# Performance work log

Measured on AMD Instinct MI355X. Metric: run time of the kernel, lower is better.

Reference implementation:

```python
import jax, jax.numpy as jnp
import numpy as np

NUM_SCALES = 7
WEIGHTS = [1.0] * 7


def get_m(r, c):
    # r, c: [B, H, W] float coords; density map is [B, a, a], a = min(H, W)
    B, H, W = r.shape
    a = min(H, W)
    N = H * W
    xf = jnp.clip(jnp.floor(r), 0, a - 1).astype(jnp.int32)
    yf = jnp.clip(jnp.floor(c), 0, a - 1).astype(jnp.int32)
    xc = jnp.clip(jnp.ceil(r), 0, a - 1).astype(jnp.int32)
    yc = jnp.clip(jnp.ceil(c), 0, a - 1).astype(jnp.int32)
    xw = r - xf.astype(r.dtype)
    yw = c - yf.astype(c.dtype)
    w_tl = (1 - xw) * (1 - yw)
    w_tr = xw * (1 - yw)
    w_bl = (1 - xw) * yw
    w_br = xw * yw
    idx = jnp.concatenate([
        (xf * a + yf).reshape(B, N), (xc * a + yf).reshape(B, N),
        (xf * a + yc).reshape(B, N), (xc * a + yc).reshape(B, N)], axis=1)
    w = jnp.concatenate([
        w_tl.reshape(B, N), w_tr.reshape(B, N),
        w_bl.reshape(B, N), w_br.reshape(B, N)], axis=1)
    dm = jnp.zeros((B, a * a), dtype=r.dtype)
    dm = dm.at[jnp.arange(B)[:, None], idx].add(w)
    return dm.reshape(B, a, a)


def masked_bce(pred, tgt):
    # torch F.binary_cross_entropy clamps log terms at -100
    p = pred.reshape(-1)
    t = tgt.reshape(-1)
    log_p = jnp.clip(jnp.log(p), -100.0, None)
    log_1mp = jnp.clip(jnp.log(1.0 - p), -100.0, None)
    bce = -(t * log_p + (1.0 - t) * log_1mp)
    valid = (t == 1.0).astype(p.dtype)
    return jnp.sum(bce * valid) / jnp.sum(valid)


def _multiscale_loss(r3, c3, r4, c4, target):
    B = target.shape[0]
    Ht, Wt = target.shape[2], target.shape[3]
    total = 0.0
    for i in range(NUM_SCALES):
        cm = get_m(r3[i], c3[i]) + get_m(r4[i], c4[i])
        cm = cm / cm.max()
        resized = jax.image.resize(cm[:, None, :, :], (B, 1, Ht, Wt), method='linear')
        total = total + WEIGHTS[i] * masked_bce(resized, target)
    return total


def setup_inputs() -> dict:
    key = jax.random.key(0)
    k1, k2, k3, k4, k5 = jax.random.split(key, 5)
    a = 512
    shp = (NUM_SCALES, 8, a, a)
    scale = float(a - 1)
    r3 = jax.random.uniform(k1, shp, dtype=jnp.float32) * scale
    c3 = jax.random.uniform(k2, shp, dtype=jnp.float32) * scale
    r4 = jax.random.uniform(k3, shp, dtype=jnp.float32) * scale
    c4 = jax.random.uniform(k4, shp, dtype=jnp.float32) * scale
    target = (jax.random.uniform(k5, (8, 1, a, a)) < 0.5).astype(jnp.float32)
    return {"r3": r3, "c3": c3, "r4": r4, "c4": c4, "target": target}


def reference(r3, c3, r4, c4, target):
    return _multiscale_loss(r3, c3, r4, c4, target)
```

## Files before the change

### kernel.cpp

```cpp
#include <hip/hip_runtime.h>
#include <math.h>

#define A      512
#define NB     8
#define NS     7
#define AA     (A*A)
#define PPS    (NB*AA)
#define RPS    15
#define NSTRIP 35
#define LROWS  16
#define NIMG   (NS*NB)
#define NBKT   (NIMG*NSTRIP)
#define CAP    16896
#define BIN_THR 256
#define PTS_PER_BLOCK 4096
#define SPLAT_THR 512
#define SCALE_F   33554432.0f
#define INV_SCALE (1.0f/33554432.0f)
#define MAXB   1024
#define BCEB   2048

#define MAXP_OFF_F 2048
#define BCEP_OFF_F 16384
#define DM_OFF_F   32768
#define BKT_OFF    ((size_t)DM_OFF_F * 4 + (size_t)NS * PPS * 4)
#define PER_IMG_B  ((size_t)NSTRIP * CAP * 8)

__global__ void init_kernel(float* __restrict__ ws) {
    if (blockIdx.x == 0) {
        for (int i = threadIdx.x; i < 2048; i += 128) ws[i] = 0.f;
        return;
    }
    int bkt = blockIdx.x - 1;
    int img = bkt / NSTRIP, k = bkt % NSTRIP;
    float4* row = (float4*)(ws + DM_OFF_F + (size_t)img * AA + (k * RPS) * A);
    row[threadIdx.x] = make_float4(0, 0, 0, 0);
}

__global__ void __launch_bounds__(BIN_THR)
bin_kernel(const float4* __restrict__ r3, const float4* __restrict__ c3,
           const float4* __restrict__ r4, const float4* __restrict__ c4,
           unsigned* __restrict__ cursors, float2* __restrict__ buckets,
           int img0) {
    const int limg = blockIdx.y;
    const int img  = img0 + limg;
    const float4* rp = blockIdx.z ? r4 : r3;
    const float4* cp = blockIdx.z ? c4 : c3;
    const int qbase = img * (AA / 4) + blockIdx.x * (PTS_PER_BLOCK / 4);

    float4 r[4], c[4];
#pragma unroll
    for (int j = 0; j < 4; j++) {
        int q = qbase + j * BIN_THR + threadIdx.x;
        r[j] = rp[q]; c[j] = cp[q];
    }

    __shared__ unsigned lcur[NSTRIP], lbase[NSTRIP];
    if (threadIdx.x < NSTRIP) lcur[threadIdx.x] = 0;
    __syncthreads();

    unsigned slot[16];
#define ALLOC(idx, rv) slot[idx] = atomicAdd(&lcur[(int)(rv) / RPS], 1u)
#pragma unroll
    for (int j = 0; j < 4; j++) {
        ALLOC(j * 4 + 0, r[j].x); ALLOC(j * 4 + 1, r[j].y);
        ALLOC(j * 4 + 2, r[j].z); ALLOC(j * 4 + 3, r[j].w);
    }
#undef ALLOC
    __syncthreads();

    if (threadIdx.x < NSTRIP)
        lbase[threadIdx.x] =
            atomicAdd(&cursors[img * NSTRIP + threadIdx.x], lcur[threadIdx.x]);
    __syncthreads();

    const int lbkt0 = limg * NSTRIP;
#define EMIT(idx, rv, cv) {                                                   \
        int s = (int)(rv) / RPS;                                              \
        unsigned sl = lbase[s] + slot[idx];                                   \
        if (sl < CAP)                                                         \
            buckets[(size_t)(lbkt0 + s) * CAP + sl] = make_float2(rv, cv); }
#pragma unroll
    for (int j = 0; j < 4; j++) {
        EMIT(j * 4 + 0, r[j].x, c[j].x); EMIT(j * 4 + 1, r[j].y, c[j].y);
        EMIT(j * 4 + 2, r[j].z, c[j].z); EMIT(j * 4 + 3, r[j].w, c[j].w);
    }
#undef EMIT
}

__device__ __forceinline__ void splat_pt(unsigned long long cp[2][LROWS][A/2],
                                         int g0, float r, float c) {
    int xf = (int)r, yf = (int)c;
    float xw = r - (float)xf, yw = c - (float)yf;
    float omx = 1.f - xw, omy = 1.f - yw;
    unsigned q0 = (unsigned)(omx * omy * SCALE_F + 0.5f);
    unsigned q1 = (unsigned)(omx * yw  * SCALE_F + 0.5f);
    unsigned q2 = (unsigned)(xw  * omy * SCALE_F + 0.5f);
    unsigned q3 = (unsigned)(xw  * yw  * SCALE_F + 0.5f);
    int lr = xf - g0, sel = yf & 1, pp = yf >> 1;
    atomicAdd(&cp[sel][lr    ][pp], ((unsigned long long)q1 << 32) | q0);
    atomicAdd(&cp[sel][lr + 1][pp], ((unsigned long long)q3 << 32) | q2);
}

__global__ void __launch_bounds__(SPLAT_THR)
splat_dense(const float2* __restrict__ buckets, const unsigned* __restrict__ cursors,
            float* __restrict__ dm, int img0) {
    __shared__ unsigned long long cp[2][LROWS][A / 2];
    const int lbkt = blockIdx.x;
    const int limg = lbkt / NSTRIP, k = lbkt % NSTRIP;
    const int img  = img0 + limg;
    const int g0   = k * RPS;

    unsigned long long* z = &cp[0][0][0];
    for (int i = threadIdx.x; i < 2 * LROWS * (A / 2); i += SPLAT_THR) z[i] = 0ull;
    __syncthreads();

    unsigned n = cursors[img * NSTRIP + k]; if (n > CAP) n = CAP;
    const float4* bp4 = (const float4*)(buckets + (size_t)lbkt * CAP);
    unsigned n2 = (n + 1) >> 1;
    for (unsigned i = threadIdx.x; i < n2; i += SPLAT_THR) {
        float4 q = bp4[i];
        splat_pt(cp, g0, q.x, q.y);
        if (2 * i + 1 < n) splat_pt(cp, g0, q.z, q.w);
    }
    __syncthreads();

    float* dimg = dm + (size_t)img * AA;
    for (int u = threadIdx.x; u < LROWS * (A / 4); u += SPLAT_THR) {
        int j = u >> 7, c4 = (u & 127) << 2, gr = g0 + j;
        if (gr >= A) continue;
        float v[4];
#pragma unroll
        for (int t = 0; t < 4; t++) {
            int cc = c4 + t;
            unsigned long long e = cp[0][j][cc >> 1];
            unsigned s = (cc & 1) ? (unsigned)(e >> 32) : (unsigned)e;
            if (cc & 1) s += (unsigned)cp[1][j][cc >> 1];
            else if (cc >= 2) s += (unsigned)(cp[1][j][(cc >> 1) - 1] >> 32);
            v[t] = (float)s * INV_SCALE;
        }
        float* dst = dimg + gr * A + c4;
        if (j == 0 || j == RPS) {
            unsafeAtomicAdd(dst + 0, v[0]); unsafeAtomicAdd(dst + 1, v[1]);
            unsafeAtomicAdd(dst + 2, v[2]); unsafeAtomicAdd(dst + 3, v[3]);
        } else {
            *(float4*)dst = make_float4(v[0], v[1], v[2], v[3]);
        }
    }
}

__device__ __forceinline__ void splat_lds_f(float lds[LROWS][A], int g0, unsigned k,
                                            float r, float c) {
    int xf = (int)r;
    if ((unsigned)xf / RPS != k) return;
    int yf = (int)c;
    float xw = r - (float)xf, yw = c - (float)yf;
    float omx = 1.f - xw, omy = 1.f - yw;
    int lr = xf - g0;
    atomicAdd(&lds[lr    ][yf    ], omx * omy);
    atomicAdd(&lds[lr + 1][yf    ], xw  * omy);
    atomicAdd(&lds[lr    ][yf + 1], omx * yw);
    atomicAdd(&lds[lr + 1][yf + 1], xw  * yw);
}

__global__ void __launch_bounds__(SPLAT_THR)
splat_gather(const float4* __restrict__ r3, const float4* __restrict__ c3,
             const float4* __restrict__ r4, const float4* __restrict__ c4,
             float* __restrict__ dm) {
    __shared__ float lds[LROWS][A];
    const unsigned k = blockIdx.x;
    const int img = blockIdx.y, tid = threadIdx.x, g0 = (int)k * RPS;
    float4* l4 = (float4*)&lds[0][0];
    for (int i = tid; i < LROWS * A / 4; i += SPLAT_THR) l4[i] = make_float4(0, 0, 0, 0);
    __syncthreads();
    const int qbase = img * (AA / 4);
    for (int i = tid; i < AA / 4; i += SPLAT_THR) {
        float4 ra = r3[qbase + i], ca = c3[qbase + i];
        float4 rb = r4[qbase + i], cb = c4[qbase + i];
        splat_lds_f(lds, g0, k, ra.x, ca.x); splat_lds_f(lds, g0, k, ra.y, ca.y);
        splat_lds_f(lds, g0, k, ra.z, ca.z); splat_lds_f(lds, g0, k, ra.w, ca.w);
        splat_lds_f(lds, g0, k, rb.x, cb.x); splat_lds_f(lds, g0, k, rb.y, cb.y);
        splat_lds_f(lds, g0, k, rb.z, cb.z); splat_lds_f(lds, g0, k, rb.w, cb.w);
    }
    __syncthreads();
    float* dimg = dm + (size_t)img * AA;
    for (int u = tid; u < LROWS * (A / 4); u += SPLAT_THR) {
        int j = u >> 7, cq = u & 127, gr = g0 + j;
        if (gr >= A) continue;
        float4 v = ((float4*)&lds[j][0])[cq];
        float* dst = dimg + gr * A + cq * 4;
        if (j == 0 || j == RPS) {
            unsafeAtomicAdd(dst + 0, v.x); unsafeAtomicAdd(dst + 1, v.y);
            unsafeAtomicAdd(dst + 2, v.z); unsafeAtomicAdd(dst + 3, v.w);
        } else {
            *(float4*)dst = v;
        }
    }
}

__global__ void max_kernel(const float4* __restrict__ dm, float* __restrict__ maxp) {
    int s = blockIdx.y;
    const float4* p = dm + (size_t)s * (PPS / 4);
    float m = 0.f;
    for (int i = blockIdx.x * blockDim.x + threadIdx.x; i < PPS / 4;
         i += gridDim.x * blockDim.x) {
        float4 v = p[i];
        m = fmaxf(m, fmaxf(fmaxf(v.x, v.y), fmaxf(v.z, v.w)));
    }
    for (int off = 32; off > 0; off >>= 1) m = fmaxf(m, __shfl_down(m, off));
    __shared__ float sm[4];
    if ((threadIdx.x & 63) == 0) sm[threadIdx.x >> 6] = m;
    __syncthreads();
    if (threadIdx.x == 0)
        maxp[s * MAXB + blockIdx.x] = fmaxf(fmaxf(sm[0], sm[1]), fmaxf(sm[2], sm[3]));
}

__global__ void max2_kernel(const float* __restrict__ maxp, float* __restrict__ mx) {
    int s = blockIdx.x;
    float m = 0.f;
    for (int i = threadIdx.x; i < MAXB; i += 256) m = fmaxf(m, maxp[s * MAXB + i]);
    for (int off = 32; off > 0; off >>= 1) m = fmaxf(m, __shfl_down(m, off));
    __shared__ float sm[4];
    if ((threadIdx.x & 63) == 0) sm[threadIdx.x >> 6] = m;
    __syncthreads();
    if (threadIdx.x == 0)
        mx[s] = fmaxf(fmaxf(sm[0], sm[1]), fmaxf(sm[2], sm[3]));
}

__global__ void __launch_bounds__(256)
bce_kernel(const float4* __restrict__ dm, const float4* __restrict__ tgt,
           const float* __restrict__ mx, float* __restrict__ bcep) {
    float lm[NS];
#pragma unroll
    for (int s = 0; s < NS; s++) lm[s] = __logf(mx[s]);
    float acc[NS];
#pragma unroll
    for (int s = 0; s < NS; s++) acc[s] = 0.f;
    float count = 0.f;
    const int NQ = PPS / 4;
    for (int i = blockIdx.x * blockDim.x + threadIdx.x; i < NQ;
         i += gridDim.x * blockDim.x) {
        float4 t = tgt[i];
        float vx = (t.x == 1.f) ? 1.f : 0.f;
        float vy = (t.y == 1.f) ? 1.f : 0.f;
        float vz = (t.z == 1.f) ? 1.f : 0.f;
        float vw = (t.w == 1.f) ? 1.f : 0.f;
        count += vx + vy + vz + vw;
#pragma unroll
        for (int s = 0; s < NS; s++) {
            float4 d = dm[s * NQ + i];
            acc[s] -= fmaxf(__logf(d.x) - lm[s], -100.f) * vx;
            acc[s] -= fmaxf(__logf(d.y) - lm[s], -100.f) * vy;
            acc[s] -= fmaxf(__logf(d.z) - lm[s], -100.f) * vz;
            acc[s] -= fmaxf(__logf(d.w) - lm[s], -100.f) * vw;
        }
    }
    for (int off = 32; off > 0; off >>= 1) {
#pragma unroll
        for (int s = 0; s < NS; s++) acc[s] += __shfl_down(acc[s], off);
        count += __shfl_down(count, off);
    }
    __shared__ float sred[4][NS + 1];
    int lane = threadIdx.x & 63, w = threadIdx.x >> 6;
    if (lane == 0) {
#pragma unroll
        for (int s = 0; s < NS; s++) sred[w][s] = acc[s];
        sred[w][NS] = count;
    }
    __syncthreads();
    if (threadIdx.x == 0) {
        for (int ww = 1; ww < 4; ww++) {
#pragma unroll
            for (int s = 0; s < NS; s++) acc[s] += sred[ww][s];
            count += sred[ww][NS];
        }
#pragma unroll
        for (int s = 0; s < NS; s++) bcep[blockIdx.x * 8 + s] = acc[s];
        bcep[blockIdx.x * 8 + NS] = count;
    }
}

__global__ void final_kernel(const float* __restrict__ bcep, float* __restrict__ out) {
    float acc[8];
#pragma unroll
    for (int c = 0; c < 8; c++) acc[c] = 0.f;
    for (int row = threadIdx.x; row < BCEB; row += 256) {
#pragma unroll
        for (int c = 0; c < 8; c++) acc[c] += bcep[row * 8 + c];
    }
    for (int off = 32; off > 0; off >>= 1) {
#pragma unroll
        for (int c = 0; c < 8; c++) acc[c] += __shfl_down(acc[c], off);
    }
    __shared__ float sred[4][8];
    int lane = threadIdx.x & 63, w = threadIdx.x >> 6;
    if (lane == 0) {
#pragma unroll
        for (int c = 0; c < 8; c++) sred[w][c] = acc[c];
    }
    __syncthreads();
    if (threadIdx.x == 0) {
        for (int ww = 1; ww < 4; ww++)
#pragma unroll
            for (int c = 0; c < 8; c++) acc[c] += sred[ww][c];
        float t = 0.f;
        for (int s = 0; s < NS; s++) t += acc[s] / acc[NS];
        out[0] = t;
    }
}

extern "C" void kernel_launch(void* const* d_in, const int* in_sizes, int n_in,
                              void* d_out, int out_size, void* d_ws, size_t ws_size,
                              hipStream_t stream) {
    const float* r3  = (const float*)d_in[0];
    const float* c3  = (const float*)d_in[1];
    const float* r4  = (const float*)d_in[2];
    const float* c4  = (const float*)d_in[3];
    const float* tgt = (const float*)d_in[4];
    float* out = (float*)d_out;

    float* ws         = (float*)d_ws;
    float* mx         = ws;
    unsigned* cursors = (unsigned*)d_ws + 16;
    float* maxp       = ws + MAXP_OFF_F;
    float* bcep       = ws + BCEP_OFF_F;
    float* dm         = ws + DM_OFF_F;

    size_t avail = (ws_size > BKT_OFF) ? ws_size - BKT_OFF : 0;
    int P = (int)(avail / PER_IMG_B);
    if (P > NIMG) P = NIMG;

    if (P >= 6) {
        float2* buckets = (float2*)((char*)d_ws + BKT_OFF);
        init_kernel<<<NBKT + 1, 128, 0, stream>>>(ws);
        for (int img0 = 0; img0 < NIMG; img0 += P) {
            int pc = NIMG - img0; if (pc > P) pc = P;
            bin_kernel<<<dim3(AA / PTS_PER_BLOCK, pc, 2), BIN_THR, 0, stream>>>(
                (const float4*)r3, (const float4*)c3,
                (const float4*)r4, (const float4*)c4, cursors, buckets, img0);
            splat_dense<<<pc * NSTRIP, SPLAT_THR, 0, stream>>>(
                buckets, cursors, dm, img0);
        }
    } else {
        hipMemsetAsync(d_ws, 0, 8192, stream);
        hipMemsetAsync(dm, 0, (size_t)NS * PPS * sizeof(float), stream);
        splat_gather<<<dim3(NSTRIP, NIMG), SPLAT_THR, 0, stream>>>(
            (const float4*)r3, (const float4*)c3,
            (const float4*)r4, (const float4*)c4, dm);
    }

    max_kernel<<<dim3(MAXB, NS), 256, 0, stream>>>((const float4*)dm, maxp);
    max2_kernel<<<NS, 256, 0, stream>>>(maxp, mx);
    bce_kernel<<<BCEB, 256, 0, stream>>>((const float4*)dm, (const float4*)tgt,
                                         mx, bcep);
    final_kernel<<<1, 256, 0, stream>>>(bcep, out);
}
```

Baseline: 370.5 us.

## Fuse max and masked BCE into splat epilogue, skip dense map write

The splat kernel now reduces interior rows directly from shared memory into per-strip partial sums of log values, valid counts and maxima, and writes only the two boundary rows of each strip to the global density map. A small cleanup kernel handles the boundary rows and counts valid targets. The final kernel then applies the max normalisation algebraically: log(v/max) = log v - log max. This removes the full write and re-read of the 7x8x512x512 density map and the separate max and BCE passes. The cost is per-block reductions and target reads inside splat, and results that depend on log(0) and clamping being reproduced through the v>0 branch plus the -100 term.

Measured after the change: 417.1 us. +12.6%, slower.

```diff
diff --git a/kernel.cpp b/kernel.cpp
--- a/kernel.cpp
+++ b/kernel.cpp
@@ -20,9 +20,11 @@
 #define MAXB   1024
 #define BCEB   2048
 
-#define MAXP_OFF_F 2048
-#define BCEP_OFF_F 16384
-#define DM_OFF_F   32768
+#define PARTS_OFF_F  2048
+#define PARTS2_OFF_F 12288
+#define NVAL_OFF_F   12800
+#define BCEP_OFF_F   16384
+#define DM_OFF_F     32768
 #define BKT_OFF    ((size_t)DM_OFF_F * 4 + (size_t)NS * PPS * 4)
 #define PER_IMG_B  ((size_t)NSTRIP * CAP * 8)
 
@@ -102,13 +104,29 @@
     atomicAdd(&cp[sel][lr + 1][pp], ((unsigned long long)q3 << 32) | q2);
 }
 
+__device__ __forceinline__ void combine4(unsigned long long cp[2][LROWS][A/2],
+                                         int j, int c4, float v[4]) {
+#pragma unroll
+    for (int t = 0; t < 4; t++) {
+        int cc = c4 + t;
+        unsigned long long e = cp[0][j][cc >> 1];
+        unsigned s = (cc & 1) ? (unsigned)(e >> 32) : (unsigned)e;
+        if (cc & 1) s += (unsigned)cp[1][j][cc >> 1];
+        else if (cc >= 2) s += (unsigned)(cp[1][j][(cc >> 1) - 1] >> 32);
+        v[t] = (float)s * INV_SCALE;
+    }
+}
+
 __global__ void __launch_bounds__(SPLAT_THR)
 splat_dense(const float2* __restrict__ buckets, const unsigned* __restrict__ cursors,
-            float* __restrict__ dm, int img0) {
+            float* __restrict__ dm, const float4* __restrict__ tgt,
+            float4* __restrict__ parts, int img0) {
     __shared__ unsigned long long cp[2][LROWS][A / 2];
+    __shared__ float sr[8][3];
     const int lbkt = blockIdx.x;
     const int limg = lbkt / NSTRIP, k = lbkt % NSTRIP;
     const int img  = img0 + limg;
+    const int b    = img & 7;
     const int g0   = k * RPS;
 
     unsigned long long* z = &cp[0][0][0];
@@ -126,26 +144,130 @@
     __syncthreads();
 
     float* dimg = dm + (size_t)img * AA;
-    for (int u = threadIdx.x; u < LROWS * (A / 4); u += SPLAT_THR) {
-        int j = u >> 7, c4 = (u & 127) << 2, gr = g0 + j;
+    for (int u = threadIdx.x; u < 2 * (A / 4); u += SPLAT_THR) {
+        int j = (u >= (A / 4)) ? RPS : 0;
+        int c4 = (u & (A / 4 - 1)) << 2;
+        int gr = g0 + j;
         if (gr >= A) continue;
         float v[4];
-#pragma unroll
-        for (int t = 0; t < 4; t++) {
-            int cc = c4 + t;
-            unsigned long long e = cp[0][j][cc >> 1];
-            unsigned s = (cc & 1) ? (unsigned)(e >> 32) : (unsigned)e;
-            if (cc & 1) s += (unsigned)cp[1][j][cc >> 1];
-            else if (cc >= 2) s += (unsigned)(cp[1][j][(cc >> 1) - 1] >> 32);
-            v[t] = (float)s * INV_SCALE;
-        }
+        combine4(cp, j, c4, v);
         float* dst = dimg + gr * A + c4;
-        if (j == 0 || j == RPS) {
-            unsafeAtomicAdd(dst + 0, v[0]); unsafeAtomicAdd(dst + 1, v[1]);
-            unsafeAtomicAdd(dst + 2, v[2]); unsafeAtomicAdd(dst + 3, v[3]);
-        } else {
-            *(float4*)dst = make_float4(v[0], v[1], v[2], v[3]);
-        }
+        unsafeAtomicAdd(dst + 0, v[0]); unsafeAtomicAdd(dst + 1, v[1]);
+        unsafeAtomicAdd(dst + 2, v[2]); unsafeAtomicAdd(dst + 3, v[3]);
+    }
+
+    float S = 0.f, Np = 0.f, mxv = 0.f;
+    const float4* timg = tgt + (size_t)b * (AA / 4);
+    for (int u = threadIdx.x; u < (RPS - 1) * (A / 4); u += SPLAT_THR) {
+        int j = 1 + (u >> 7), cq = u & 127, gr = g0 + j;
+        if (gr >= A) continue;
+        float v[4];
+        combine4(cp, j, cq << 2, v);
+        mxv = fmaxf(mxv, fmaxf(fmaxf(v[0], v[1]), fmaxf(v[2], v[3])));
+        float4 t = timg[gr * (A / 4) + cq];
+        if (t.x == 1.f && v[0] > 0.f) { S += __logf(v[0]); Np += 1.f; }
+        if (t.y == 1.f && v[1] > 0.f) { S += __logf(v[1]); Np += 1.f; }
+        if (t.z == 1.f && v[2] > 0.f) { S += __logf(v[2]); Np += 1.f; }
+        if (t.w == 1.f && v[3] > 0.f) { S += __logf(v[3]); Np += 1.f; }
+    }
+    for (int off = 32; off > 0; off >>= 1) {
+        S += __shfl_down(S, off); Np += __shfl_down(Np, off);
+        mxv = fmaxf(mxv, __shfl_down(mxv, off));
+    }
+    int lane = threadIdx.x & 63, w = threadIdx.x >> 6;
+    if (lane == 0) { sr[w][0] = S; sr[w][1] = Np; sr[w][2] = mxv; }
+    __syncthreads();
+    if (threadIdx.x == 0) {
+        for (int ww = 1; ww < 8; ww++) {
+            S += sr[ww][0]; Np += sr[ww][1]; mxv = fmaxf(mxv, sr[ww][2]);
+        }
+        parts[img * NSTRIP + k] = make_float4(S, Np, mxv, 0.f);
+    }
+}
+
+__global__ void __launch_bounds__(256)
+cleanup_kernel(const float* __restrict__ dm, const float4* __restrict__ tgt,
+               float4* __restrict__ parts2, float* __restrict__ nval) {
+    const int bx = blockIdx.x;
+    float a0 = 0.f, a1 = 0.f, a2 = 0.f;
+    if (bx < NIMG) {
+        const int img = bx, b = img & 7;
+        const float4* dimg = (const float4*)(dm + (size_t)img * AA);
+        const float4* timg = tgt + (size_t)b * (AA / 4);
+        for (int u = threadIdx.x; u < NSTRIP * (A / 4); u += 256) {
+            int kk = u >> 7, cq = u & 127, gr = kk * RPS;
+            float4 d = dimg[gr * (A / 4) + cq];
+            float4 t = timg[gr * (A / 4) + cq];
+            a2 = fmaxf(a2, fmaxf(fmaxf(d.x, d.y), fmaxf(d.z, d.w)));
+            if (t.x == 1.f && d.x > 0.f) { a0 += __logf(d.x); a1 += 1.f; }
+            if (t.y == 1.f && d.y > 0.f) { a0 += __logf(d.y); a1 += 1.f; }
+            if (t.z == 1.f && d.z > 0.f) { a0 += __logf(d.z); a1 += 1.f; }
+            if (t.w == 1.f && d.w > 0.f) { a0 += __logf(d.w); a1 += 1.f; }
+        }
+    } else {
+        const float4* timg = tgt + (size_t)(bx - NIMG) * (AA / 4);
+        for (int u = threadIdx.x; u < AA / 4; u += 256) {
+            float4 t = timg[u];
+            a0 += ((t.x == 1.f) ? 1.f : 0.f) + ((t.y == 1.f) ? 1.f : 0.f) +
+                  ((t.z == 1.f) ? 1.f : 0.f) + ((t.w == 1.f) ? 1.f : 0.f);
+        }
+    }
+    for (int off = 32; off > 0; off >>= 1) {
+        a0 += __shfl_down(a0, off); a1 += __shfl_down(a1, off);
+        a2 = fmaxf(a2, __shfl_down(a2, off));
+    }
+    __shared__ float sr[4][3];
+    int lane = threadIdx.x & 63, w = threadIdx.x >> 6;
+    if (lane == 0) { sr[w][0] = a0; sr[w][1] = a1; sr[w][2] = a2; }
+    __syncthreads();
+    if (threadIdx.x == 0) {
+        for (int ww = 1; ww < 4; ww++) {
+            a0 += sr[ww][0]; a1 += sr[ww][1]; a2 = fmaxf(a2, sr[ww][2]);
+        }
+        if (bx < NIMG) parts2[bx] = make_float4(a0, a1, a2, 0.f);
+        else           nval[bx - NIMG] = a0;
+    }
+}
+
+__global__ void __launch_bounds__(256)
+final_fused(const float4* __restrict__ parts, const float4* __restrict__ parts2,
+            const float* __restrict__ nval, float* __restrict__ out) {
+    __shared__ float red[4][3];
+    __shared__ float ps[NS][3];
+    const int lane = threadIdx.x & 63, w = threadIdx.x >> 6;
+    for (int s = 0; s < NS; s++) {
+        float S = 0.f, Np = 0.f, Mx = 0.f;
+        for (int t = threadIdx.x; t < NB * NSTRIP; t += 256) {
+            float4 p = parts[s * NB * NSTRIP + t];
+            S += p.x; Np += p.y; Mx = fmaxf(Mx, p.z);
+        }
+        if (threadIdx.x < NB) {
+            float4 p = parts2[s * NB + threadIdx.x];
+            S += p.x; Np += p.y; Mx = fmaxf(Mx, p.z);
+        }
+        for (int off = 32; off > 0; off >>= 1) {
+            S += __shfl_down(S, off); Np += __shfl_down(Np, off);
+            Mx = fmaxf(Mx, __shfl_down(Mx, off));
+        }
+        if (lane == 0) { red[w][0] = S; red[w][1] = Np; red[w][2] = Mx; }
+        __syncthreads();
+        if (threadIdx.x == 0) {
+            for (int ww = 1; ww < 4; ww++) {
+                S += red[ww][0]; Np += red[ww][1]; Mx = fmaxf(Mx, red[ww][2]);
+            }
+            ps[s][0] = S; ps[s][1] = Np; ps[s][2] = Mx;
+        }
+        __syncthreads();
+    }
+    if (threadIdx.x == 0) {
+        float Nv = 0.f;
+        for (int b = 0; b < NB; b++) Nv += nval[b];
+        float t = 0.f;
+        for (int s = 0; s < NS; s++) {
+            float lm = __logf(ps[s][2]);
+            t += (ps[s][1] * lm - ps[s][0] + 100.f * (Nv - ps[s][1])) / Nv;
+        }
+        out[0] = t;
     }
 }
 
@@ -322,7 +444,10 @@
     float* ws         = (float*)d_ws;
     float* mx         = ws;
     unsigned* cursors = (unsigned*)d_ws + 16;
-    float* maxp       = ws + MAXP_OFF_F;
+    float4* parts     = (float4*)(ws + PARTS_OFF_F);
+    float4* parts2    = (float4*)(ws + PARTS2_OFF_F);
+    float* nval       = ws + NVAL_OFF_F;
+    float* maxp       = ws + PARTS_OFF_F;
     float* bcep       = ws + BCEP_OFF_F;
     float* dm         = ws + DM_OFF_F;
 
@@ -339,19 +464,21 @@
                 (const float4*)r3, (const float4*)c3,
                 (const float4*)r4, (const float4*)c4, cursors, buckets, img0);
             splat_dense<<<pc * NSTRIP, SPLAT_THR, 0, stream>>>(
-                buckets, cursors, dm, img0);
-        }
+                buckets, cursors, dm, (const float4*)tgt, parts, img0);
+        }
+        cleanup_kernel<<<NIMG + NB, 256, 0, stream>>>(
+            dm, (const float4*)tgt, parts2, nval);
+        final_fused<<<1, 256, 0, stream>>>(parts, parts2, nval, out);
     } else {
         hipMemsetAsync(d_ws, 0, 8192, stream);
         hipMemsetAsync(dm, 0, (size_t)NS * PPS * sizeof(float), stream);
         splat_gather<<<dim3(NSTRIP, NIMG), SPLAT_THR, 0, stream>>>(
             (const float4*)r3, (const float4*)c3,
             (const float4*)r4, (const float4*)c4, dm);
-    }
-
-    max_kernel<<<dim3(MAXB, NS), 256, 0, stream>>>((const float4*)dm, maxp);
-    max2_kernel<<<NS, 256, 0, stream>>>(maxp, mx);
-    bce_kernel<<<BCEB, 256, 0, stream>>>((const float4*)dm, (const float4*)tgt,
-                                         mx, bcep);
-    final_kernel<<<1, 256, 0, stream>>>(bcep, out);
-}
+        max_kernel<<<dim3(MAXB, NS), 256, 0, stream>>>((const float4*)dm, maxp);
+        max2_kernel<<<NS, 256, 0, stream>>>(maxp, mx);
+        bce_kernel<<<BCEB, 256, 0, stream>>>((const float4*)dm, (const float4*)tgt,
+                                             mx, bcep);
+        final_kernel<<<1, 256, 0, stream>>>(bcep, out);
+    }
+}
```
